# Kernel optimization log

Measured on AMD Instinct MI355X. Metric: run time of the kernel, lower is better.

## Reference

```python
import jax, jax.numpy as jnp
import numpy as np

B, S, D, H, E, K = 2, 2048, 1024, 4096, 8, 2


def setup_inputs() -> dict:
    key = jax.random.key(0)
    ks = jax.random.split(key, 5)
    x = jax.random.normal(ks[0], (B, S, D), dtype=jnp.float32)
    W = 0.02 * jax.random.normal(ks[1], (H, D), dtype=jnp.float32)
    bias = 0.02 * jax.random.normal(ks[2], (H,), dtype=jnp.float32)
    # alpha initialized near 1 (nn.Parameter(torch.ones(...)) + learned perturbation)
    alpha = 1.0 + 0.02 * jax.random.normal(ks[3], (E, D), dtype=jnp.float32)
    beta = 0.02 * jax.random.normal(ks[4], (E, D), dtype=jnp.float32)
    return {"x": x, "W": W, "bias": bias, "alpha": alpha, "beta": beta}


def reference(x, W, bias, alpha, beta):
    """MoEXLayer eval-mode forward (sparsity-aware routing + expert combine).

    x: [B,S,D], W: [H,D], bias: [H], alpha/beta: [E,D]. Returns [B,S,H].
    """
    E = alpha.shape[0]
    # --- Router: per-virtual-expert Gaussian pre-activation statistics ---
    # reconstructed_weight(alpha, beta) = W * alpha + beta  (column-wise affine)
    W_rec = W[None, :, :] * alpha[:, None, :] + beta[:, None, :]      # [E,H,D]
    mu_w = W_rec.mean(axis=1)                                          # [E,D]
    var_w = W_rec.var(axis=1)                                          # [E,D] (unbiased=False)
    mu_h = jnp.einsum('bsd,ed->bse', x, mu_w) + bias.mean()            # [B,S,E]
    sigma_h = jnp.sqrt(jnp.einsum('bsd,ed->bse', x * x, var_w) + 1e-8) # [B,S,E]
    router_logits = jax.lax.erf(mu_h / (jnp.sqrt(2.0) * sigma_h))      # [B,S,E]

    # --- Top-k routing: softmax over top-k logits, zeros elsewhere ---
    topk_vals, topk_idx = jax.lax.top_k(router_logits, K)              # [B,S,K]
    topk_w = jax.nn.softmax(topk_vals, axis=-1)                        # [B,S,K]
    router_weights = (jax.nn.one_hot(topk_idx, E, dtype=x.dtype)
                      * topk_w[..., None]).sum(axis=-2)                # [B,S,E]

    # --- Expert compute + combine (dispatch passes alpha only => beta=0) ---
    W_disp = W[None, :, :] * alpha[:, None, :]                         # [E,H,D]
    pre = jnp.einsum('bsd,ehd->bseh', x, W_disp) + bias                # [B,S,E,H]
    expert_out = jax.nn.relu(pre)
    out = jnp.einsum('bseh,bse->bsh', expert_out, router_weights)      # [B,S,H]
    return out
```

## Files before the change

kernel.cpp:

```cpp
#include <hip/hip_runtime.h>
#include <hip/hip_bf16.h>
#include <math.h>

#define DD 1024
#define HH 4096
#define EE 8
#define MTOK 4096
#define MROWS 8192

typedef __attribute__((ext_vector_type(8))) short bf16x8;
typedef __attribute__((ext_vector_type(4))) float f32x4;

__device__ __forceinline__ unsigned short f2bf(float x){
  __hip_bfloat16 h = __float2bfloat16(x);
  return *reinterpret_cast<unsigned short*>(&h);
}

__device__ __forceinline__ void gload16(const void* g, void* l){
  __builtin_amdgcn_global_load_lds((__attribute__((address_space(1))) void*)g,
                                   (__attribute__((address_space(3))) void*)l,
                                   16, 0, 0);
}

__global__ void cvtstats_kernel(const float4* __restrict__ W4, ushort4* __restrict__ Wb4,
                                float* __restrict__ pmean, float* __restrict__ pm2){
  int rc = blockIdx.x;
  int tid = threadIdx.x;
  double s0=0,s1=0,s2_=0,s3=0, q0=0,q1=0,q2=0,q3=0;
  for (int h = rc * 32; h < rc * 32 + 32; ++h){
    float4 w = W4[(size_t)h * 256 + tid];
    Wb4[(size_t)h * 256 + tid] = make_ushort4(f2bf(w.x), f2bf(w.y), f2bf(w.z), f2bf(w.w));
    s0 += w.x; q0 += (double)w.x * w.x;
    s1 += w.y; q1 += (double)w.y * w.y;
    s2_ += w.z; q2 += (double)w.z * w.z;
    s3 += w.w; q3 += (double)w.w * w.w;
  }
  int d0 = rc * DD + tid * 4;
  pmean[d0]   = (float)s0;  pm2[d0]   = (float)q0;
  pmean[d0+1] = (float)s1;  pm2[d0+1] = (float)q1;
  pmean[d0+2] = (float)s2_; pm2[d0+2] = (float)q2;
  pmean[d0+3] = (float)s3;  pm2[d0+3] = (float)q3;
}

__global__ void colstats_final_kernel(const float* __restrict__ pmean,
                                      const float* __restrict__ pm2,
                                      double* __restrict__ cmean, double* __restrict__ cvar){
  int d = blockIdx.x * 256 + threadIdx.x;
  double s = 0.0, s2 = 0.0;
  for (int c = 0; c < 128; ++c){ s += (double)pmean[c * DD + d]; s2 += (double)pm2[c * DD + d]; }
  double m = s / (double)HH;
  cmean[d] = m;
  cvar[d]  = s2 / (double)HH - m * m;
}

__global__ void biasmean_kernel(const float* __restrict__ bias, double* __restrict__ bmean){
  __shared__ double red[256];
  double s = 0.0;
  for (int h = threadIdx.x; h < HH; h += 256) s += (double)bias[h];
  red[threadIdx.x] = s;
  __syncthreads();
  for (int k = 128; k > 0; k >>= 1){
    if (threadIdx.x < k) red[threadIdx.x] += red[threadIdx.x + k];
    __syncthreads();
  }
  if (threadIdx.x == 0) *bmean = red[0] / (double)HH;
}

__global__ void muvw_kernel(const float* __restrict__ alpha, const float* __restrict__ beta,
                            const double* __restrict__ cmean, const double* __restrict__ cvar,
                            float* __restrict__ muw, float* __restrict__ vw){
  int i = blockIdx.x * 256 + threadIdx.x;
  int d = i & (DD - 1);
  double a = (double)alpha[i];
  muw[i] = (float)(a * cmean[d] + (double)beta[i]);
  vw[i]  = (float)(a * a * cvar[d]);
}

__global__ __launch_bounds__(256) void router_kernel(const float4* __restrict__ x4,
                                                     const float4* __restrict__ alpha4,
                                                     const float4* __restrict__ muw4,
                                                     const float4* __restrict__ vw4,
                                                     const double* __restrict__ bmeanp,
                                                     unsigned short* __restrict__ Xs,
                                                     float2* __restrict__ wpair){
  int wv = threadIdx.x >> 6, lane = threadIdx.x & 63;
  int t = blockIdx.x * 4 + wv;
  const float4* xt = x4 + (size_t)t * 256;

  float4 xv[4];
  double mu[EE], s2[EE];
  #pragma unroll
  for (int e = 0; e < EE; ++e){ mu[e] = 0.0; s2[e] = 0.0; }

  #pragma unroll
  for (int r = 0; r < 4; ++r){
    int c = lane + 64 * r;
    float4 xf = xt[c];
    xv[r] = xf;
    float x2x = xf.x * xf.x, x2y = xf.y * xf.y, x2z = xf.z * xf.z, x2w = xf.w * xf.w;
    #pragma unroll
    for (int e = 0; e < EE; ++e){
      float4 m4 = muw4[e * 256 + c];
      float4 v4 = vw4[e * 256 + c];
      mu[e] += (double)xf.x * m4.x + (double)xf.y * m4.y
             + (double)xf.z * m4.z + (double)xf.w * m4.w;
      s2[e] += (double)x2x * v4.x + (double)x2y * v4.y
             + (double)x2z * v4.z + (double)x2w * v4.w;
    }
  }

  #pragma unroll
  for (int off = 32; off > 0; off >>= 1){
    #pragma unroll
    for (int e = 0; e < EE; ++e){
      mu[e] += __shfl_xor(mu[e], off);
      s2[e] += __shfl_xor(s2[e], off);
    }
  }

  double bm = *bmeanp;
  double z[EE];
  #pragma unroll
  for (int e = 0; e < EE; ++e){
    double m = mu[e] + bm;
    double v = s2[e] + 1e-8;
    z[e] = m / sqrt(2.0 * v);
  }
  int e1 = 0;
  #pragma unroll
  for (int e = 1; e < EE; ++e) if (z[e] > z[e1]) e1 = e;
  int e2 = -1;
  #pragma unroll
  for (int e = 0; e < EE; ++e){
    if (e == e1) continue;
    if (e2 < 0 || z[e] > z[e2]) e2 = e;
  }
  double lg1 = erf(z[e1]), lg2 = erf(z[e2]);
  double ex = exp(lg2 - lg1);
  float w1 = (float)(1.0 / (1.0 + ex));
  float w2 = (float)(ex / (1.0 + ex));
  if (lane == 0) wpair[t] = make_float2(w1, w2);

  const float4* a1 = alpha4 + (size_t)e1 * 256;
  const float4* a2 = alpha4 + (size_t)e2 * 256;
  ushort4* X1 = (ushort4*)(Xs + (size_t)(2 * t) * DD);
  ushort4* X2 = (ushort4*)(Xs + (size_t)(2 * t + 1) * DD);
  #pragma unroll
  for (int r = 0; r < 4; ++r){
    int c = lane + 64 * r;
    float4 xf = xv[r];
    float4 av = a1[c];
    X1[c] = make_ushort4(f2bf(xf.x * av.x), f2bf(xf.y * av.y),
                         f2bf(xf.z * av.z), f2bf(xf.w * av.w));
    av = a2[c];
    X2[c] = make_ushort4(f2bf(xf.x * av.x), f2bf(xf.y * av.y),
                         f2bf(xf.z * av.z), f2bf(xf.w * av.w));
  }
}

#define BM 256
#define BN 256
#define BKT 64
#define NKT (DD / BKT)
#define ASLOT (BM * BKT)
#define BSLOT (BN * BKT)

__global__ __launch_bounds__(512, 2) void gemm_kernel(const unsigned short* __restrict__ Xs,
                                                      const unsigned short* __restrict__ Wb,
                                                      const float* __restrict__ bias,
                                                      const float2* __restrict__ wpair,
                                                      float* __restrict__ out){
  __shared__ __align__(16) unsigned short As[2 * ASLOT];
  __shared__ __align__(16) unsigned short Bs[2 * BSLOT];

  int tid = threadIdx.x, lane = tid & 63, wv = tid >> 6;
  int wr = wv >> 2, wc = wv & 3;
  int l15 = lane & 15;

  int bid = blockIdx.x;
  int ch = bid & 7, local = bid >> 3;
  int mtile = ch * 4 + (local & 3);
  int ntile = local >> 2;
  int bm0 = mtile * BM, bn0 = ntile * BN;

  int sr = tid >> 3;
  int sc = tid & 7;
  int scg = sc ^ (sr & 7);
  const unsigned short* gA = Xs + (size_t)(bm0 + sr) * DD + scg * 8;
  const unsigned short* gB = Wb + (size_t)(bn0 + sr) * DD + scg * 8;
  unsigned short* lA = As + tid * 8;
  unsigned short* lB = Bs + tid * 8;

  auto stage = [&](int kt, int slot){
    int koff = kt * BKT;
    #pragma unroll
    for (int j = 0; j < 4; ++j)
      gload16(gA + (size_t)(64 * j) * DD + koff, lA + slot * ASLOT + j * (64 * BKT));
    #pragma unroll
    for (int j = 0; j < 4; ++j)
      gload16(gB + (size_t)(64 * j) * DD + koff, lB + slot * BSLOT + j * (64 * BKT));
  };

  int x7 = l15 & 7;
  int chk0 = (lane >> 4) ^ x7;
  int chk1 = (4 + (lane >> 4)) ^ x7;
  const unsigned short* Arow = As + (wr * 128 + l15) * BKT;
  const unsigned short* Brow = Bs + (wc * 64 + l15) * BKT;

  f32x4 acc[8][4] = {};
  bf16x8 afr[4], bfr[4];

  stage(0, 0);
  stage(1, 1);
  asm volatile("s_waitcnt vmcnt(8)" ::: "memory");
  __builtin_amdgcn_s_barrier();

  #define PHASE(MH, CHK, READB, LGKM)                                            \
    {                                                                            \
      if (READB){                                                                \
        _Pragma("unroll")                                                        \
        for (int ni = 0; ni < 4; ++ni)                                           \
          bfr[ni] = *(const bf16x8*)(Bb1 + ni * (16 * BKT) + (CHK) * 8);         \
      }                                                                          \
      _Pragma("unroll")                                                          \
      for (int i = 0; i < 4; ++i)                                                \
        afr[i] = *(const bf16x8*)(Ab1 + ((MH) * 4 + i) * (16 * BKT) + (CHK) * 8);\
      __builtin_amdgcn_s_barrier();                                              \
      __builtin_amdgcn_s_setprio(1);                                             \
      _Pragma("unroll")                                                          \
      for (int mi = 0; mi < 4; ++mi)                                             \
        _Pragma("unroll")                                                        \
        for (int ni = 0; ni < 4; ++ni)                                           \
          acc[(MH) * 4 + mi][ni] =                                               \
            __builtin_amdgcn_mfma_f32_16x16x32_bf16(afr[mi], bfr[ni],            \
                                                    acc[(MH) * 4 + mi][ni], 0, 0, 0); \
      __builtin_amdgcn_s_setprio(0);                                             \
      if (LGKM) asm volatile("s_waitcnt lgkmcnt(0)" ::: "memory");               \
      __builtin_amdgcn_s_barrier();                                              \
    }

  #pragma unroll 1
  for (int kt = 0; kt < NKT; ++kt){
    int slot = kt & 1;
    const unsigned short* Ab1 = Arow + slot * ASLOT;
    const unsigned short* Bb1 = Brow + slot * BSLOT;
    PHASE(0, chk0, 1, 0)
    PHASE(1, chk0, 0, 0)
    PHASE(0, chk1, 1, 0)
    PHASE(1, chk1, 0, 1)
    if (kt + 2 < NKT) stage(kt + 2, slot);
    if (kt + 1 < NKT){
      if (kt + 2 < NKT) asm volatile("s_waitcnt vmcnt(8)" ::: "memory");
      else              asm volatile("s_waitcnt vmcnt(0)" ::: "memory");
      __builtin_amdgcn_s_barrier();
    }
  }
  #undef PHASE

  #pragma unroll
  for (int mi = 0; mi < 8; ++mi){
    int rbase = bm0 + wr * 128 + mi * 16 + ((lane >> 4) << 2);
    #pragma unroll
    for (int jp = 0; jp < 2; ++jp){
      int gm = rbase + jp * 2;
      int t = gm >> 1;
      float2 w = wpair[t];
      #pragma unroll
      for (int ni = 0; ni < 4; ++ni){
        int gh = bn0 + wc * 64 + ni * 16 + l15;
        float bz = bias[gh];
        float v0 = acc[mi][ni][jp * 2]     + bz;
        float v1 = acc[mi][ni][jp * 2 + 1] + bz;
        out[(size_t)t * HH + gh] = w.x * fmaxf(v0, 0.f) + w.y * fmaxf(v1, 0.f);
      }
    }
  }
}

extern "C" void kernel_launch(void* const* d_in, const int* in_sizes, int n_in,
                              void* d_out, int out_size, void* d_ws, size_t ws_size,
                              hipStream_t stream) {
  const float* x     = (const float*)d_in[0];
  const float* W     = (const float*)d_in[1];
  const float* bias  = (const float*)d_in[2];
  const float* alpha = (const float*)d_in[3];
  const float* beta  = (const float*)d_in[4];
  float* out = (float*)d_out;

  char* ws = (char*)d_ws;
  unsigned short* Wb = (unsigned short*)ws;
  unsigned short* Xs = (unsigned short*)(ws + (8u << 20));
  float2* wpair      = (float2*)(ws + (24u << 20));
  double* cmean      = (double*)(ws + (24u << 20) + (64u << 10));
  double* cvar       = cmean + DD;
  double* bmean      = cvar + DD;
  float* pmean       = (float*)(ws + (24u << 20) + (128u << 10));
  float* pm2         = pmean + 128 * DD;
  float* muw         = (float*)(ws + (26u << 20));
  float* vw          = muw + EE * DD;

  cvtstats_kernel<<<128, 256, 0, stream>>>((const float4*)W, (ushort4*)Wb, pmean, pm2);
  colstats_final_kernel<<<4, 256, 0, stream>>>(pmean, pm2, cmean, cvar);
  biasmean_kernel<<<1, 256, 0, stream>>>(bias, bmean);
  muvw_kernel<<<32, 256, 0, stream>>>(alpha, beta, cmean, cvar, muw, vw);
  router_kernel<<<MTOK / 4, 256, 0, stream>>>((const float4*)x, (const float4*)alpha,
                                              (const float4*)muw, (const float4*)vw,
                                              bmean, Xs, wpair);
  gemm_kernel<<<(MROWS / BM) * (HH / BN), 512, 0, stream>>>(Xs, Wb, bias, wpair, out);
}
```

Measured before the change: 126.4 us.

## Fuse router prep kernels and simplify GEMM main loop to single-barrier double buffer

Three small preprocessing kernels (column stats finalize, bias mean, mu/var weights) are merged into one launch to cut launch overhead. The GEMM main loop drops the four-phase interleaved schedule with a prefetch distance of two and per-phase barriers. It now prefetches only the next tile, loads all eight A fragments and four B fragments per k-substep, and issues 32 MFMAs back to back. Launch bounds move from 2 to 1 blocks per CU, which frees registers for the larger fragment set but may reduce latency hiding and overlap of loads with compute.

```diff
diff --git a/kernel.cpp b/kernel.cpp
--- a/kernel.cpp
+++ b/kernel.cpp
@@ -42,38 +42,37 @@
   pmean[d0+3] = (float)s3;  pm2[d0+3] = (float)q3;
 }
 
-__global__ void colstats_final_kernel(const float* __restrict__ pmean,
-                                      const float* __restrict__ pm2,
-                                      double* __restrict__ cmean, double* __restrict__ cvar){
-  int d = blockIdx.x * 256 + threadIdx.x;
+__global__ void finalize_kernel(const float* __restrict__ pmean, const float* __restrict__ pm2,
+                                const float* __restrict__ bias,
+                                const float* __restrict__ alpha, const float* __restrict__ beta,
+                                double* __restrict__ bmean,
+                                float* __restrict__ muw, float* __restrict__ vw){
+  int tid = threadIdx.x;
+  int d = blockIdx.x * 256 + tid;
   double s = 0.0, s2 = 0.0;
   for (int c = 0; c < 128; ++c){ s += (double)pmean[c * DD + d]; s2 += (double)pm2[c * DD + d]; }
   double m = s / (double)HH;
-  cmean[d] = m;
-  cvar[d]  = s2 / (double)HH - m * m;
-}
-
-__global__ void biasmean_kernel(const float* __restrict__ bias, double* __restrict__ bmean){
-  __shared__ double red[256];
-  double s = 0.0;
-  for (int h = threadIdx.x; h < HH; h += 256) s += (double)bias[h];
-  red[threadIdx.x] = s;
-  __syncthreads();
-  for (int k = 128; k > 0; k >>= 1){
-    if (threadIdx.x < k) red[threadIdx.x] += red[threadIdx.x + k];
+  double v = s2 / (double)HH - m * m;
+
+  #pragma unroll
+  for (int e = 0; e < EE; ++e){
+    double a = (double)alpha[e * DD + d];
+    muw[e * DD + d] = (float)(a * m + (double)beta[e * DD + d]);
+    vw[e * DD + d]  = (float)(a * a * v);
+  }
+
+  if (blockIdx.x == 0){
+    __shared__ double red[256];
+    double bs = 0.0;
+    for (int h = tid; h < HH; h += 256) bs += (double)bias[h];
+    red[tid] = bs;
     __syncthreads();
-  }
-  if (threadIdx.x == 0) *bmean = red[0] / (double)HH;
-}
-
-__global__ void muvw_kernel(const float* __restrict__ alpha, const float* __restrict__ beta,
-                            const double* __restrict__ cmean, const double* __restrict__ cvar,
-                            float* __restrict__ muw, float* __restrict__ vw){
-  int i = blockIdx.x * 256 + threadIdx.x;
-  int d = i & (DD - 1);
-  double a = (double)alpha[i];
-  muw[i] = (float)(a * cmean[d] + (double)beta[i]);
-  vw[i]  = (float)(a * a * cvar[d]);
+    for (int k = 128; k > 0; k >>= 1){
+      if (tid < k) red[tid] += red[tid + k];
+      __syncthreads();
+    }
+    if (tid == 0) *bmean = red[0] / (double)HH;
+  }
 }
 
 __global__ __launch_bounds__(256) void router_kernel(const float4* __restrict__ x4,
@@ -162,16 +161,15 @@
 #define BN 256
 #define BKT 64
 #define NKT (DD / BKT)
-#define ASLOT (BM * BKT)
-#define BSLOT (BN * BKT)
-
-__global__ __launch_bounds__(512, 2) void gemm_kernel(const unsigned short* __restrict__ Xs,
+#define ASZ (BM * BKT)
+
+__global__ __launch_bounds__(512, 1) void gemm_kernel(const unsigned short* __restrict__ Xs,
                                                       const unsigned short* __restrict__ Wb,
                                                       const float* __restrict__ bias,
                                                       const float2* __restrict__ wpair,
                                                       float* __restrict__ out){
-  __shared__ __align__(16) unsigned short As[2 * ASLOT];
-  __shared__ __align__(16) unsigned short Bs[2 * BSLOT];
+  __shared__ __align__(16) unsigned short As[2 * ASZ];
+  __shared__ __align__(16) unsigned short Bs[2 * ASZ];
 
   int tid = threadIdx.x, lane = tid & 63, wv = tid >> 6;
   int wr = wv >> 2, wc = wv & 3;
@@ -195,67 +193,57 @@
     int koff = kt * BKT;
     #pragma unroll
     for (int j = 0; j < 4; ++j)
-      gload16(gA + (size_t)(64 * j) * DD + koff, lA + slot * ASLOT + j * (64 * BKT));
+      gload16(gA + (size_t)(64 * j) * DD + koff, lA + slot * ASZ + j * 4096);
     #pragma unroll
     for (int j = 0; j < 4; ++j)
-      gload16(gB + (size_t)(64 * j) * DD + koff, lB + slot * BSLOT + j * (64 * BKT));
+      gload16(gB + (size_t)(64 * j) * DD + koff, lB + slot * ASZ + j * 4096);
   };
 
-  int x7 = l15 & 7;
-  int chk0 = (lane >> 4) ^ x7;
-  int chk1 = (4 + (lane >> 4)) ^ x7;
-  const unsigned short* Arow = As + (wr * 128 + l15) * BKT;
-  const unsigned short* Brow = Bs + (wc * 64 + l15) * BKT;
+  int r7 = l15 & 7;
+  int posr0 = (lane >> 4) ^ r7;
+  int posr1 = (4 + (lane >> 4)) ^ r7;
 
   f32x4 acc[8][4] = {};
-  bf16x8 afr[4], bfr[4];
 
   stage(0, 0);
-  stage(1, 1);
-  asm volatile("s_waitcnt vmcnt(8)" ::: "memory");
-  __builtin_amdgcn_s_barrier();
-
-  #define PHASE(MH, CHK, READB, LGKM)                                            \
-    {                                                                            \
-      if (READB){                                                                \
-        _Pragma("unroll")                                                        \
-        for (int ni = 0; ni < 4; ++ni)                                           \
-          bfr[ni] = *(const bf16x8*)(Bb1 + ni * (16 * BKT) + (CHK) * 8);         \
-      }                                                                          \
-      _Pragma("unroll")                                                          \
-      for (int i = 0; i < 4; ++i)                                                \
-        afr[i] = *(const bf16x8*)(Ab1 + ((MH) * 4 + i) * (16 * BKT) + (CHK) * 8);\
-      __builtin_amdgcn_s_barrier();                                              \
-      __builtin_amdgcn_s_setprio(1);                                             \
-      _Pragma("unroll")                                                          \
-      for (int mi = 0; mi < 4; ++mi)                                             \
-        _Pragma("unroll")                                                        \
-        for (int ni = 0; ni < 4; ++ni)                                           \
-          acc[(MH) * 4 + mi][ni] =                                               \
-            __builtin_amdgcn_mfma_f32_16x16x32_bf16(afr[mi], bfr[ni],            \
-                                                    acc[(MH) * 4 + mi][ni], 0, 0, 0); \
-      __builtin_amdgcn_s_setprio(0);                                             \
-      if (LGKM) asm volatile("s_waitcnt lgkmcnt(0)" ::: "memory");               \
-      __builtin_amdgcn_s_barrier();                                              \
-    }
-
   #pragma unroll 1
-  for (int kt = 0; kt < NKT; ++kt){
-    int slot = kt & 1;
-    const unsigned short* Ab1 = Arow + slot * ASLOT;
-    const unsigned short* Bb1 = Brow + slot * BSLOT;
-    PHASE(0, chk0, 1, 0)
-    PHASE(1, chk0, 0, 0)
-    PHASE(0, chk1, 1, 0)
-    PHASE(1, chk1, 0, 1)
-    if (kt + 2 < NKT) stage(kt + 2, slot);
-    if (kt + 1 < NKT){
-      if (kt + 2 < NKT) asm volatile("s_waitcnt vmcnt(8)" ::: "memory");
-      else              asm volatile("s_waitcnt vmcnt(0)" ::: "memory");
-      __builtin_amdgcn_s_barrier();
-    }
-  }
-  #undef PHASE
+  for (int t = 0; t < NKT; ++t){
+    int slot = t & 1;
+    if (t < NKT - 1){
+      stage(t + 1, slot ^ 1);
+      asm volatile("s_waitcnt vmcnt(8)" ::: "memory");
+    } else {
+      asm volatile("s_waitcnt vmcnt(0)" ::: "memory");
+    }
+    __builtin_amdgcn_s_barrier();
+
+    const unsigned short* Ab = As + slot * ASZ;
+    const unsigned short* Bb = Bs + slot * ASZ;
+
+    #pragma unroll
+    for (int ks = 0; ks < 2; ++ks){
+      int pos = ks ? posr1 : posr0;
+      bf16x8 af[8], bfr[4];
+      #pragma unroll
+      for (int mi = 0; mi < 8; ++mi)
+        af[mi] = *(const bf16x8*)(Ab + (wr * 128 + mi * 16 + l15) * BKT + pos * 8);
+      #pragma unroll
+      for (int ni = 0; ni < 4; ++ni)
+        bfr[ni] = *(const bf16x8*)(Bb + (wc * 64 + ni * 16 + l15) * BKT + pos * 8);
+
+      __builtin_amdgcn_s_setprio(1);
+      #pragma unroll
+      for (int ni = 0; ni < 4; ++ni)
+        #pragma unroll
+        for (int mi = 0; mi < 8; ++mi)
+          acc[mi][ni] = __builtin_amdgcn_mfma_f32_16x16x32_bf16(af[mi], bfr[ni],
+                                                               acc[mi][ni], 0, 0, 0);
+      __builtin_amdgcn_s_setprio(0);
+    }
+
+    asm volatile("s_waitcnt lgkmcnt(0)" ::: "memory");
+    __builtin_amdgcn_s_barrier();
+  }
 
   #pragma unroll
   for (int mi = 0; mi < 8; ++mi){
@@ -263,15 +251,15 @@
     #pragma unroll
     for (int jp = 0; jp < 2; ++jp){
       int gm = rbase + jp * 2;
-      int t = gm >> 1;
-      float2 w = wpair[t];
+      int tt = gm >> 1;
+      float2 w = wpair[tt];
       #pragma unroll
       for (int ni = 0; ni < 4; ++ni){
         int gh = bn0 + wc * 64 + ni * 16 + l15;
         float bz = bias[gh];
         float v0 = acc[mi][ni][jp * 2]     + bz;
         float v1 = acc[mi][ni][jp * 2 + 1] + bz;
-        out[(size_t)t * HH + gh] = w.x * fmaxf(v0, 0.f) + w.y * fmaxf(v1, 0.f);
+        out[(size_t)tt * HH + gh] = w.x * fmaxf(v0, 0.f) + w.y * fmaxf(v1, 0.f);
       }
     }
   }
@@ -291,18 +279,14 @@
   unsigned short* Wb = (unsigned short*)ws;
   unsigned short* Xs = (unsigned short*)(ws + (8u << 20));
   float2* wpair      = (float2*)(ws + (24u << 20));
-  double* cmean      = (double*)(ws + (24u << 20) + (64u << 10));
-  double* cvar       = cmean + DD;
-  double* bmean      = cvar + DD;
+  double* bmean      = (double*)(ws + (24u << 20) + (64u << 10));
   float* pmean       = (float*)(ws + (24u << 20) + (128u << 10));
   float* pm2         = pmean + 128 * DD;
   float* muw         = (float*)(ws + (26u << 20));
   float* vw          = muw + EE * DD;
 
   cvtstats_kernel<<<128, 256, 0, stream>>>((const float4*)W, (ushort4*)Wb, pmean, pm2);
-  colstats_final_kernel<<<4, 256, 0, stream>>>(pmean, pm2, cmean, cvar);
-  biasmean_kernel<<<1, 256, 0, stream>>>(bias, bmean);
-  muvw_kernel<<<32, 256, 0, stream>>>(alpha, beta, cmean, cvar, muw, vw);
+  finalize_kernel<<<4, 256, 0, stream>>>(pmean, pm2, bias, alpha, beta, bmean, muw, vw);
   router_kernel<<<MTOK / 4, 256, 0, stream>>>((const float4*)x, (const float4*)alpha,
                                               (const float4*)muw, (const float4*)vw,
                                               bmean, Xs, wpair);
```

New measurement: 115.5 us. 1.09x faster.
